# Kernel optimization log

Hardware: AMD Instinct MI355X
Metric: run time of the kernel (lower is better)

## Reference

```python
import jax, jax.numpy as jnp
import numpy as np

E = 1024  # embed_dim
H = 16    # heads
D = E // H            # head_dim = 64
M = 4 * D             # nb_features = 256
B, N = 4, 4096
KERNEL_EPS = 1e-4


def setup_inputs() -> dict:
    key = jax.random.key(0)
    ks = jax.random.split(key, 7)
    s = E ** -0.5
    return {
        "x": jax.random.normal(ks[0], (B, N, E), jnp.float32),
        "Wq": jax.random.normal(ks[1], (E, E), jnp.float32) * s,
        "bq": jnp.zeros((E,), jnp.float32),
        "Wk": jax.random.normal(ks[2], (E, E), jnp.float32) * s,
        "bk": jnp.zeros((E,), jnp.float32),
        "Wv": jax.random.normal(ks[3], (E, E), jnp.float32) * s,
        "bv": jnp.zeros((E,), jnp.float32),
        "Wo": jax.random.normal(ks[4], (E, E), jnp.float32) * s,
        "bo": jnp.zeros((E,), jnp.float32),
        "proj": jax.random.normal(ks[5], (M, D), jnp.float32),  # FAVOR+ random features
    }


def softmax_kernel(data, proj, is_query):
    # data: [B,H,N,D], proj: [M,D] -> features [B,H,N,M]
    d = data.shape[-1]
    data_n = data * (d ** -0.25)
    ratio = proj.shape[0] ** -0.5
    dd = jnp.einsum('bhnd,md->bhnm', data_n, proj)
    diag = 0.5 * jnp.sum(data_n * data_n, axis=-1, keepdims=True)
    if is_query:
        stab = jnp.max(dd, axis=-1, keepdims=True)
    else:
        stab = jnp.max(dd)
    return ratio * (jnp.exp(dd - diag - stab) + KERNEL_EPS)


def reference(x, Wq, bq, Wk, bk, Wv, bv, Wo, bo, proj):
    b, n, e = x.shape
    def split_heads(t):
        return t.reshape(b, n, H, D).transpose(0, 2, 1, 3)  # [B,H,N,D]
    q = split_heads(x @ Wq.T + bq)
    k = split_heads(x @ Wk.T + bk)
    v = split_heads(x @ Wv.T + bv)

    qf = softmax_kernel(q, proj, is_query=True)   # [B,H,N,M]
    kf = softmax_kernel(k, proj, is_query=False)  # [B,H,N,M]

    # non-causal linear attention: O(N*M*D)
    k_sum = jnp.sum(kf, axis=-2)                          # [B,H,M]
    d_inv = 1.0 / jnp.einsum('bhnm,bhm->bhn', qf, k_sum)  # [B,H,N]
    context = jnp.einsum('bhnm,bhnd->bhmd', kf, v)        # [B,H,M,D]
    out = jnp.einsum('bhnm,bhmd,bhn->bhnd', qf, context, d_inv)

    out = out.transpose(0, 2, 1, 3).reshape(b, n, e)
    return out @ Wo.T + bo
```

## Files before the change

### kernel.cpp

```cpp
#include <hip/hip_runtime.h>
#include <hip/hip_bf16.h>
#include <stdint.h>


#define TOKN  16384
#define SEQ   4096
#define EMB   1024
#define LDQ   3072
#define NHEAD 16
#define HD    64
#define NF    256
#define BHN   64

static __device__ __forceinline__ constexpr float c1f()  { return 0.35355339059327379f; }
static __device__ __forceinline__ constexpr float ratf() { return 0.0625f; }
static __device__ __forceinline__ constexpr float kepsf(){ return 1e-4f; }

typedef unsigned short u16;
typedef unsigned int   u32;
typedef __attribute__((ext_vector_type(8))) short bf16x8;
typedef __attribute__((ext_vector_type(4))) float f32x4;
typedef __attribute__((ext_vector_type(4))) u16   u16x4;

union U8 { bf16x8 v8; u16x4 q[2]; };

__device__ __forceinline__ float bf2f(u16 u) { return __uint_as_float(((u32)u) << 16); }
__device__ __forceinline__ u16 f2bf(float f) {
  u32 u = __float_as_uint(f);
  u += 0x7fffu + ((u >> 16) & 1u);
  return (u16)(u >> 16);
}
__device__ __forceinline__ u32 encf(float f) {
  u32 u = __float_as_uint(f);
  return (u & 0x80000000u) ? ~u : (u | 0x80000000u);
}
__device__ __forceinline__ float decf(u32 e) {
  u32 u = (e & 0x80000000u) ? (e & 0x7fffffffu) : ~e;
  return __uint_as_float(u);
}

__device__ __forceinline__ void gl2lds16(const u16* g, void* l) {
  __builtin_amdgcn_global_load_lds(
      (const __attribute__((address_space(1))) u32*)g,
      (__attribute__((address_space(3))) u32*)l, 16, 0, 0);
}

#define ZERO_ACC(acc)                         \
  _Pragma("unroll") for (int _i = 0; _i < 4; _i++) \
  _Pragma("unroll") for (int _j = 0; _j < 4; _j++) acc[_i][_j] = (f32x4)0.0f;

template <int BM, int BN>
__device__ __forceinline__ void gemm_core(const u16* __restrict__ Ag, long lda,
                                          const u16* __restrict__ Bg, long ldb,
                                          int K, u16* sA, u16* sB,
                                          f32x4 (&acc)[4][4]) {
  const int tid = threadIdx.x;
  const int w = tid >> 6, l = tid & 63;
  constexpr int WM = BM / 64;
  const int wm = w % WM, wn = w / WM;
  const int lrow = l & 15, g4 = l >> 4;
  constexpr int AI = (BM * 8) / 256;
  constexpr int BI = (BN * 8) / 256;

  for (int k0 = 0; k0 < K; k0 += 64) {
    __syncthreads();
#pragma unroll
    for (int i = 0; i < AI; i++) {
      int q = i * 256 + tid;
      int row = q >> 3, part = (q & 7) ^ (row & 7);
      gl2lds16(Ag + (long)row * lda + k0 + part * 8,
               (char*)sA + i * 4096 + w * 1024);
    }
#pragma unroll
    for (int i = 0; i < BI; i++) {
      int q = i * 256 + tid;
      int row = q >> 3, part = (q & 7) ^ (row & 7);
      gl2lds16(Bg + (long)row * ldb + k0 + part * 8,
               (char*)sB + i * 4096 + w * 1024);
    }
    __syncthreads();
#pragma unroll
    for (int kk = 0; kk < 2; kk++) {
      bf16x8 af[4], bfr[4];
#pragma unroll
      for (int mt = 0; mt < 4; mt++) {
        int row = wm * 64 + mt * 16 + lrow;
        af[mt] = *(const bf16x8*)(sA + row * 64 + (((kk * 4 + g4) ^ (row & 7)) * 8));
      }
#pragma unroll
      for (int nt = 0; nt < 4; nt++) {
        int row = wn * 64 + nt * 16 + lrow;
        bfr[nt] = *(const bf16x8*)(sB + row * 64 + (((kk * 4 + g4) ^ (row & 7)) * 8));
      }
#pragma unroll
      for (int mt = 0; mt < 4; mt++)
#pragma unroll
        for (int nt = 0; nt < 4; nt++)
          acc[mt][nt] = __builtin_amdgcn_mfma_f32_16x16x32_bf16(af[mt], bfr[nt], acc[mt][nt], 0, 0, 0);
    }
  }
}

template <bool BF16OUT>
__global__ __launch_bounds__(256) void k_gemm(const u16* __restrict__ A, const u16* __restrict__ Bw,
                                              void* __restrict__ Cout, const float* __restrict__ bias,
                                              int K, int lda, int ldb, int ldc) {
  __shared__ __align__(16) u16 sA[128 * 64];
  __shared__ __align__(16) u16 sB[128 * 64];
  const int nbx = gridDim.x;
  const int nwg = nbx * gridDim.y;
  int lin = blockIdx.y * nbx + blockIdx.x;
  if ((nwg & 7) == 0) {
    int per = nwg >> 3;
    lin = (lin & 7) * per + (lin >> 3);
  }
  const int m0 = (lin / nbx) * 128, n0 = (lin % nbx) * 128;
  f32x4 acc[4][4]; ZERO_ACC(acc);
  gemm_core<128, 128>(A + (long)m0 * lda, lda, Bw + (long)n0 * ldb, ldb, K, sA, sB, acc);
  const int l = threadIdx.x & 63, w = threadIdx.x >> 6;
  const int wm = w & 1, wn = w >> 1, lr4 = (l >> 4) * 4, lc = l & 15;
#pragma unroll
  for (int nt = 0; nt < 4; nt++) {
    int gcol = n0 + wn * 64 + nt * 16 + lc;
    float bia = bias[gcol];
#pragma unroll
    for (int mt = 0; mt < 4; mt++)
#pragma unroll
      for (int r = 0; r < 4; r++) {
        int grow = m0 + wm * 64 + mt * 16 + lr4 + r;
        float v = acc[mt][nt][r] + bia;
        if (BF16OUT) ((u16*)Cout)[(long)grow * ldc + gcol] = f2bf(v);
        else         ((float*)Cout)[(long)grow * ldc + gcol] = v;
      }
  }
}

__global__ __launch_bounds__(256) void k_gemm3(const u16* __restrict__ A, const u16* __restrict__ Bw,
                                               u16* __restrict__ Cout,
                                               const float* __restrict__ b0, const float* __restrict__ b1,
                                               const float* __restrict__ b2,
                                               int K, int lda, int ldb, int ldc) {
  __shared__ __align__(16) u16 sA[128 * 64];
  __shared__ __align__(16) u16 sB[128 * 64];
  const int nbx = gridDim.x;
  const int nwg = nbx * gridDim.y;
  int lin = blockIdx.y * nbx + blockIdx.x;
  if ((nwg & 7) == 0) {
    int per = nwg >> 3;
    lin = (lin & 7) * per + (lin >> 3);
  }
  const int m0 = (lin / nbx) * 128, n0 = (lin % nbx) * 128;
  f32x4 acc[4][4]; ZERO_ACC(acc);
  gemm_core<128, 128>(A + (long)m0 * lda, lda, Bw + (long)n0 * ldb, ldb, K, sA, sB, acc);
  const int l = threadIdx.x & 63, w = threadIdx.x >> 6;
  const int wm = w & 1, wn = w >> 1, lr4 = (l >> 4) * 4, lc = l & 15;
  const int seg = n0 >> 10;
  const float* bias = seg == 0 ? b0 : (seg == 1 ? b1 : b2);
#pragma unroll
  for (int nt = 0; nt < 4; nt++) {
    int gcol = n0 + wn * 64 + nt * 16 + lc;
    float bia = bias[gcol & 1023];
#pragma unroll
    for (int mt = 0; mt < 4; mt++)
#pragma unroll
      for (int r = 0; r < 4; r++) {
        int grow = m0 + wm * 64 + mt * 16 + lr4 + r;
        Cout[(long)grow * ldc + gcol] = f2bf(acc[mt][nt][r] + bia);
      }
  }
}

__global__ __launch_bounds__(256) void k_vT(const u16* __restrict__ vb, u16* __restrict__ vT,
                                            float* __restrict__ vsum) {
  __shared__ u16 t[64][72];
  const int bh = blockIdx.y, n0 = blockIdx.x * 64, b = bh >> 4, h = bh & 15;
  const int tid = threadIdx.x;
#pragma unroll
  for (int i = 0; i < 2; i++) {
    int idx = i * 256 + tid, row = idx >> 3, c8 = idx & 7;
    U8 u;
    u.v8 = *(const bf16x8*)&vb[((long)(b * SEQ) + n0 + row) * LDQ + h * HD + c8 * 8];
    *(u16x4*)&t[row][c8 * 8]     = u.q[0];
    *(u16x4*)&t[row][c8 * 8 + 4] = u.q[1];
  }
  __syncthreads();
  const int nq = tid & 15, dh = tid >> 4;
#pragma unroll
  for (int i = 0; i < 4; i++) {
    int d = i * 16 + dh;
    u16x4 pk; float s = 0.f;
#pragma unroll
    for (int j = 0; j < 4; j++) { u16 v = t[nq * 4 + j][d]; pk[j] = v; s += bf2f(v); }
    *(u16x4*)&vT[((long)bh * HD + d) * SEQ + n0 + nq * 4] = pk;
    s += __shfl_xor(s, 1); s += __shfl_xor(s, 2);
    s += __shfl_xor(s, 4); s += __shfl_xor(s, 8);
    if (nq == 0) atomicAdd(&vsum[bh * HD + d], s);
  }
}

__global__ __launch_bounds__(256, 2) void k_fk_ctx(const u16* __restrict__ kb, const u16* __restrict__ vT,
                                                   const u16* __restrict__ projb, u16* __restrict__ part,
                                                   float* __restrict__ su, u32* __restrict__ stabEnc) {
  __shared__ __align__(16) u16 sU[4][64 * 64];
  const int ck = blockIdx.x, bh = blockIdx.y, b = bh >> 4, h = bh & 15;
  const int tid = threadIdx.x, w = tid >> 6, l = tid & 63;
  const int c = l & 15, g = l >> 4;
  u16* sUw = &sU[w][0];
  const int sw = c & 7;

  bf16x8 pf[4][2];
#pragma unroll
  for (int nt = 0; nt < 4; nt++)
#pragma unroll
    for (int k0 = 0; k0 < 2; k0++)
      pf[nt][k0] = *(const bf16x8*)&projb[(w * 64 + nt * 16 + c) * 64 + k0 * 32 + g * 8];

  f32x4 acc2[4][4]; ZERO_ACC(acc2);
  float suv[4] = {0.f, 0.f, 0.f, 0.f};
  float amax = -1e30f;
  const long tok0 = (long)b * SEQ + ck * 256;

  for (int s = 0; s < 4; s++) {
    const long t0 = tok0 + s * 64;
    bf16x8 af[4][2];
#pragma unroll
    for (int mt = 0; mt < 4; mt++)
#pragma unroll
      for (int k0 = 0; k0 < 2; k0++)
        af[mt][k0] = *(const bf16x8*)&kb[(t0 + mt * 16 + c) * LDQ + h * HD + k0 * 32 + g * 8];
    bf16x8 vf[2][4];
#pragma unroll
    for (int k0 = 0; k0 < 2; k0++)
#pragma unroll
      for (int nt = 0; nt < 4; nt++)
        vf[k0][nt] = *(const bf16x8*)&vT[((long)bh * HD + nt * 16 + c) * SEQ +
                                         ck * 256 + s * 64 + k0 * 32 + g * 8];

#pragma unroll
    for (int mt = 0; mt < 4; mt++) {
      float ss = 0.f;
#pragma unroll
      for (int k0 = 0; k0 < 2; k0++)
#pragma unroll
        for (int j = 0; j < 8; j++) {
          float v = bf2f((u16)af[mt][k0][j]);
          ss += v * v;
        }
      ss += __shfl_xor(ss, 16);
      ss += __shfl_xor(ss, 32);
      const float dgrow = ss * 0.0625f;
      f32x4 accR[4];
#pragma unroll
      for (int nt = 0; nt < 4; nt++) accR[nt] = (f32x4)0.0f;
#pragma unroll
      for (int k0 = 0; k0 < 2; k0++)
#pragma unroll
        for (int nt = 0; nt < 4; nt++)
          accR[nt] = __builtin_amdgcn_mfma_f32_16x16x32_bf16(af[mt][k0], pf[nt][k0], accR[nt], 0, 0, 0);
      float dg[4];
#pragma unroll
      for (int r = 0; r < 4; r++) dg[r] = __shfl(dgrow, g * 4 + r);
#pragma unroll
      for (int nt = 0; nt < 4; nt++) {
        u16x4 pk;
#pragma unroll
        for (int r = 0; r < 4; r++) {
          float a = accR[nt][r];
          amax = fmaxf(amax, a);
          float U = __expf(fmaf(a, c1f(), -dg[r]));
          pk[r] = f2bf(U);
          suv[nt] += U;
        }
        *(u16x4*)&sUw[(nt * 16 + c) * 64 + (((mt * 2 + (g >> 1)) ^ sw) * 2 + (g & 1)) * 4] = pk;
      }
    }
#pragma unroll
    for (int k0 = 0; k0 < 2; k0++) {
      bf16x8 uf[4];
#pragma unroll
      for (int mt = 0; mt < 4; mt++)
        uf[mt] = *(const bf16x8*)&sUw[(mt * 16 + c) * 64 + ((k0 * 4 + g) ^ sw) * 8];
#pragma unroll
      for (int mt = 0; mt < 4; mt++)
#pragma unroll
        for (int nt = 0; nt < 4; nt++)
          acc2[mt][nt] = __builtin_amdgcn_mfma_f32_16x16x32_bf16(uf[mt], vf[k0][nt], acc2[mt][nt], 0, 0, 0);
    }
  }
  const long zp = (long)(bh * 16 + ck);
#pragma unroll
  for (int mt = 0; mt < 4; mt++)
#pragma unroll
    for (int nt = 0; nt < 4; nt++)
#pragma unroll
      for (int r = 0; r < 4; r++) {
        int m = w * 64 + mt * 16 + g * 4 + r;
        int d = nt * 16 + c;
        part[(zp * NF + m) * HD + d] = f2bf(acc2[mt][nt][r]);
      }
#pragma unroll
  for (int nt = 0; nt < 4; nt++) {
    float v = suv[nt];
    v += __shfl_xor(v, 16);
    v += __shfl_xor(v, 32);
    if (l < 16) atomicAdd(&su[bh * NF + w * 64 + nt * 16 + l], v);
  }
  for (int o = 32; o; o >>= 1) amax = fmaxf(amax, __shfl_xor(amax, o));
  if (l == 0) atomicMax(stabEnc, encf(c1f() * amax));
}

__global__ __launch_bounds__(256, 4) void k_fq_attn(const u16* __restrict__ qb, const u16* __restrict__ projb,
                                                    const float* __restrict__ k_sum, const float* __restrict__ ksum_tot,
                                                    const u16* __restrict__ ct_bf, const float* __restrict__ ctsum,
                                                    u16* __restrict__ attn_bf) {
  __shared__ __align__(16) u16 sUq[64 * 256];
  __shared__ float redmax[4][64];
  __shared__ float redsum[4][64];
  const int bh = blockIdx.y, b = bh >> 4, h = bh & 15;
  const long t0 = (long)b * SEQ + blockIdx.x * 64;
  const int tid = threadIdx.x, w = tid >> 6, l = tid & 63;
  const int lrow = l & 15, lk = (l >> 4) * 8, lr4 = (l >> 4) * 4, lc = l & 15;

  bf16x8 pf[4][2];
#pragma unroll
  for (int mt = 0; mt < 4; mt++)
#pragma unroll
    for (int k0 = 0; k0 < 2; k0++)
      pf[mt][k0] = *(const bf16x8*)&projb[(w * 64 + mt * 16 + lrow) * 64 + k0 * 32 + lk];
  bf16x8 af[4][2];
#pragma unroll
  for (int nt = 0; nt < 4; nt++)
#pragma unroll
    for (int k0 = 0; k0 < 2; k0++)
      af[nt][k0] = *(const bf16x8*)&qb[(t0 + nt * 16 + lrow) * LDQ + h * HD + k0 * 32 + lk];

  float dgq[4];
#pragma unroll
  for (int nt = 0; nt < 4; nt++) {
    float ss = 0.f;
#pragma unroll
    for (int k0 = 0; k0 < 2; k0++)
#pragma unroll
      for (int j = 0; j < 8; j++) {
        float v = bf2f((u16)af[nt][k0][j]);
        ss += v * v;
      }
    ss += __shfl_xor(ss, 16);
    ss += __shfl_xor(ss, 32);
    dgq[nt] = ss * 0.0625f;
  }

  f32x4 ksr[4];
#pragma unroll
  for (int mt = 0; mt < 4; mt++)
    ksr[mt] = *(const f32x4*)&k_sum[(long)bh * NF + w * 64 + mt * 16 + lr4];

#pragma unroll
  for (int nt = 0; nt < 4; nt++) {
    f32x4 accC[4];
#pragma unroll
    for (int mt = 0; mt < 4; mt++) accC[mt] = (f32x4)0.0f;
#pragma unroll
    for (int k0 = 0; k0 < 2; k0++)
#pragma unroll
      for (int mt = 0; mt < 4; mt++)
        accC[mt] = __builtin_amdgcn_mfma_f32_16x16x32_bf16(pf[mt][k0], af[nt][k0], accC[mt], 0, 0, 0);

    const int tok = nt * 16 + lc;
    const int trow = tok * NF, tsw = tok & 7;
    float vmax = -1e30f, s = 0.f;
#pragma unroll
    for (int mt = 0; mt < 4; mt++) {
      const int fb = w * 64 + mt * 16 + lr4;
      u16x4 pk;
#pragma unroll
      for (int r = 0; r < 4; r++) {
        float dd = c1f() * accC[mt][r];
        vmax = fmaxf(vmax, dd);
        float U = __expf(dd - dgq[nt]);
        pk[r] = f2bf(U);
        s += U * ksr[mt][r];
      }
      *(u16x4*)&sUq[trow + (((fb >> 3) ^ tsw) << 3) + (fb & 7)] = pk;
    }
    vmax = fmaxf(vmax, __shfl_xor(vmax, 16));
    vmax = fmaxf(vmax, __shfl_xor(vmax, 32));
    s += __shfl_xor(s, 16);
    s += __shfl_xor(s, 32);
    if (l < 16) { redmax[w][nt * 16 + l] = vmax; redsum[w][nt * 16 + l] = s; }
  }
  __syncthreads();
  f32x4 acc2[4];
#pragma unroll
  for (int mt = 0; mt < 4; mt++) acc2[mt] = (f32x4)0.0f;
#pragma unroll
  for (int kk = 0; kk < 8; kk++) {
    bf16x8 bfr = *(const bf16x8*)&ct_bf[((long)bh * HD + w * 16 + lrow) * NF + kk * 32 + lk];
#pragma unroll
    for (int mt = 0; mt < 4; mt++) {
      int row = mt * 16 + lrow;
      bf16x8 a2 = *(const bf16x8*)&sUq[row * NF + (((kk * 4 + (l >> 4)) ^ (row & 7)) * 8)];
      acc2[mt] = __builtin_amdgcn_mfma_f32_16x16x32_bf16(a2, bfr, acc2[mt], 0, 0, 0);
    }
  }
  const float kst = ksum_tot[bh];
  const float cts = ctsum[(long)bh * HD + w * 16 + lc];
#pragma unroll
  for (int mt = 0; mt < 4; mt++)
#pragma unroll
    for (int r = 0; r < 4; r++) {
      int row = mt * 16 + lr4 + r;
      float rs = fmaxf(fmaxf(redmax[0][row], redmax[1][row]),
                       fmaxf(redmax[2][row], redmax[3][row]));
      float S1 = redsum[0][row] + redsum[1][row] + redsum[2][row] + redsum[3][row];
      float ers = __expf(-rs);
      float di = 1.0f / (ratf() * (ers * S1 + kepsf() * kst));
      float a_ = di * ratf() * ers;
      float b_ = di * ratf() * kepsf();
      float ov = a_ * acc2[mt][r] + b_ * cts;
      attn_bf[(t0 + row) * EMB + h * HD + w * 16 + lc] = f2bf(ov);
    }
}

__global__ void k_cvt(const float* __restrict__ s, u16* __restrict__ d, long n4) {
  long i = (long)blockIdx.x * blockDim.x + threadIdx.x;
  if (i >= n4) return;
  float4 v = ((const float4*)s)[i];
  u16x4 o = { f2bf(v.x), f2bf(v.y), f2bf(v.z), f2bf(v.w) };
  ((u16x4*)d)[i] = o;
}

__global__ void k_init(float* su, float* vsum, u32* stabEnc) {
  int i = blockIdx.x * 256 + threadIdx.x;
  if (i < BHN * NF) su[i] = 0.f;
  if (i < BHN * HD) vsum[i] = 0.f;
  if (i == 0) *stabEnc = 0u;
}

__global__ __launch_bounds__(256) void k_asm_ksum(const float* __restrict__ su, const u32* __restrict__ stabEnc,
                                                  float* __restrict__ k_sum, float* __restrict__ ksum_tot) {
  __shared__ float red[256];
  int z = blockIdx.x, m = threadIdx.x;
  float es = __expf(-decf(*stabEnc));
  float v = ratf() * (es * su[(long)z * NF + m] + kepsf() * (float)SEQ);
  k_sum[(long)z * NF + m] = v;
  red[m] = v;
  __syncthreads();
  for (int s = 128; s > 0; s >>= 1) {
    if (m < s) red[m] += red[m + s];
    __syncthreads();
  }
  if (m == 0) ksum_tot[z] = red[0];
}

__global__ __launch_bounds__(256) void k_asm_ct(const u16* __restrict__ part, const float* __restrict__ vsum,
                                                const u32* __restrict__ stabEnc, u16* __restrict__ ct_bf,
                                                float* __restrict__ ctsum) {
  __shared__ float red[4][64];
  const int z = blockIdx.x, tid = threadIdx.x;
  const int w = tid >> 6, l = tid & 63;
  float es = __expf(-decf(*stabEnc));
  float vs = vsum[(long)z * HD + l];
  float csum = 0.f;
  for (int m = w; m < NF; m += 4) {
    float a = 0.f;
#pragma unroll
    for (int ck = 0; ck < 16; ck++)
      a += bf2f(part[((long)(z * 16 + ck) * NF + m) * HD + l]);
    float cv = ratf() * (es * a + kepsf() * vs);
    ct_bf[((long)z * HD + l) * NF + m] = f2bf(cv);
    csum += cv;
  }
  red[w][l] = csum;
  __syncthreads();
  if (tid < 64)
    ctsum[(long)z * HD + tid] = red[0][tid] + red[1][tid] + red[2][tid] + red[3][tid];
}

extern "C" void kernel_launch(void* const* d_in, const int* in_sizes, int n_in,
                              void* d_out, int out_size, void* d_ws, size_t ws_size,
                              hipStream_t stream) {
  const float* x    = (const float*)d_in[0];
  const float* Wq   = (const float*)d_in[1];
  const float* bq   = (const float*)d_in[2];
  const float* Wk   = (const float*)d_in[3];
  const float* bk   = (const float*)d_in[4];
  const float* Wv   = (const float*)d_in[5];
  const float* bv   = (const float*)d_in[6];
  const float* Wo   = (const float*)d_in[7];
  const float* bo   = (const float*)d_in[8];
  const float* proj = (const float*)d_in[9];

  char* base = (char*)d_ws;
  size_t off = 0;
  auto alloc = [&](size_t bytes) {
    off = (off + 255) & ~(size_t)255;
    char* r = base + off;
    off += bytes;
    return r;
  };
  u16*  xb     = (u16*)alloc((size_t)TOKN * EMB * 2);
  u16*  wqkv   = (u16*)alloc((size_t)3 * EMB * EMB * 2);
  u16*  wob    = (u16*)alloc((size_t)EMB * EMB * 2);
  u16*  projb  = (u16*)alloc((size_t)NF * HD * 2);
  u16*  qkv    = (u16*)alloc((size_t)TOKN * LDQ * 2);
  float* su    = (float*)alloc((size_t)BHN * NF * 4);
  float* k_sum = (float*)alloc((size_t)BHN * NF * 4);
  float* ksum_t= (float*)alloc((size_t)BHN * 4);
  float* vsum  = (float*)alloc((size_t)BHN * HD * 4);
  float* ctsum = (float*)alloc((size_t)BHN * HD * 4);
  u32*  stabE  = (u32*)alloc(256);
  u16*  ct_bf  = (u16*)alloc((size_t)BHN * HD * NF * 2);
  u16*  qb     = qkv;
  u16*  kb     = qkv + EMB;
  u16*  vb     = qkv + 2 * EMB;
  u16*  part   = xb;
  u16*  attn_bf= xb;
  u16*  vT     = (u16*)d_out;

  k_init<<<64, 256, 0, stream>>>(su, vsum, stabE);
  k_cvt<<<(TOKN * EMB / 4 + 255) / 256, 256, 0, stream>>>(x, xb, (long)TOKN * EMB / 4);
  k_cvt<<<(EMB * EMB / 4 + 255) / 256, 256, 0, stream>>>(Wq, wqkv, (long)EMB * EMB / 4);
  k_cvt<<<(EMB * EMB / 4 + 255) / 256, 256, 0, stream>>>(Wk, wqkv + (size_t)EMB * EMB, (long)EMB * EMB / 4);
  k_cvt<<<(EMB * EMB / 4 + 255) / 256, 256, 0, stream>>>(Wv, wqkv + (size_t)2 * EMB * EMB, (long)EMB * EMB / 4);
  k_cvt<<<(EMB * EMB / 4 + 255) / 256, 256, 0, stream>>>(Wo, wob, (long)EMB * EMB / 4);
  k_cvt<<<(NF * HD / 4 + 255) / 256, 256, 0, stream>>>(proj, projb, (long)NF * HD / 4);
  k_gemm3<<<dim3(LDQ / 128, TOKN / 128), 256, 0, stream>>>(xb, wqkv, qkv, bq, bk, bv,
                                                           EMB, EMB, EMB, LDQ);
  k_vT<<<dim3(SEQ / 64, BHN), 256, 0, stream>>>(vb, vT, vsum);
  k_fk_ctx<<<dim3(16, BHN), 256, 0, stream>>>(kb, vT, projb, part, su, stabE);
  k_asm_ksum<<<BHN, 256, 0, stream>>>(su, stabE, k_sum, ksum_t);
  k_asm_ct<<<BHN, 256, 0, stream>>>(part, vsum, stabE, ct_bf, ctsum);
  k_fq_attn<<<dim3(SEQ / 64, BHN), 256, 0, stream>>>(qb, projb, k_sum, ksum_t, ct_bf, ctsum, attn_bf);
  k_gemm<false><<<dim3(EMB / 128, TOKN / 128), 256, 0, stream>>>(attn_bf, wob, d_out, bo, EMB, EMB, EMB, EMB);
}
```

Before: 513.0 us.

## Double-buffer GEMM shared-memory tiles to overlap global loads with MFMA

Converts the GEMM main loop to a two-stage LDS ping-pong: the next K-tile is issued with direct global-to-LDS loads while the current tile is consumed by MFMAs, synchronized through explicit vmcnt waits and s_barrier. This hides global-load latency that previously stalled each iteration between two syncthreads. LDS per block doubles to 64KB, which can reduce occupancy, and the hardcoded vmcnt(8) depends on exactly eight loads per thread per tile.

Result: faster. 501.9 us (-2.2%).

```diff
diff --git a/kernel.cpp b/kernel.cpp
--- a/kernel.cpp
+++ b/kernel.cpp
@@ -61,36 +61,53 @@
   const int lrow = l & 15, g4 = l >> 4;
   constexpr int AI = (BM * 8) / 256;
   constexpr int BI = (BN * 8) / 256;
-
-  for (int k0 = 0; k0 < K; k0 += 64) {
-    __syncthreads();
+  static_assert(AI + BI == 8, "vmcnt(8) literal assumes 8 loads/thread/tile");
+  constexpr int ABUF = BM * 64;
+  constexpr int BBUF = BN * 64;
+
+  auto stage = [&](int k0, int sel) {
 #pragma unroll
     for (int i = 0; i < AI; i++) {
       int q = i * 256 + tid;
       int row = q >> 3, part = (q & 7) ^ (row & 7);
       gl2lds16(Ag + (long)row * lda + k0 + part * 8,
-               (char*)sA + i * 4096 + w * 1024);
+               (char*)(sA + sel * ABUF) + i * 4096 + w * 1024);
     }
 #pragma unroll
     for (int i = 0; i < BI; i++) {
       int q = i * 256 + tid;
       int row = q >> 3, part = (q & 7) ^ (row & 7);
       gl2lds16(Bg + (long)row * ldb + k0 + part * 8,
-               (char*)sB + i * 4096 + w * 1024);
-    }
-    __syncthreads();
+               (char*)(sB + sel * BBUF) + i * 4096 + w * 1024);
+    }
+  };
+
+  stage(0, 0);
+  const int NT = K >> 6;
+  for (int t = 0; t < NT; ++t) {
+    const int sel = t & 1;
+    if (t + 1 < NT) {
+      stage((t + 1) * 64, sel ^ 1);
+      asm volatile("s_waitcnt vmcnt(8)" ::: "memory");
+    } else {
+      asm volatile("s_waitcnt vmcnt(0)" ::: "memory");
+    }
+    __builtin_amdgcn_s_barrier();
+    __builtin_amdgcn_sched_barrier(0);
+    const u16* pA = sA + sel * ABUF;
+    const u16* pB = sB + sel * BBUF;
 #pragma unroll
     for (int kk = 0; kk < 2; kk++) {
       bf16x8 af[4], bfr[4];
 #pragma unroll
       for (int mt = 0; mt < 4; mt++) {
         int row = wm * 64 + mt * 16 + lrow;
-        af[mt] = *(const bf16x8*)(sA + row * 64 + (((kk * 4 + g4) ^ (row & 7)) * 8));
+        af[mt] = *(const bf16x8*)(pA + row * 64 + (((kk * 4 + g4) ^ (row & 7)) * 8));
       }
 #pragma unroll
       for (int nt = 0; nt < 4; nt++) {
         int row = wn * 64 + nt * 16 + lrow;
-        bfr[nt] = *(const bf16x8*)(sB + row * 64 + (((kk * 4 + g4) ^ (row & 7)) * 8));
+        bfr[nt] = *(const bf16x8*)(pB + row * 64 + (((kk * 4 + g4) ^ (row & 7)) * 8));
       }
 #pragma unroll
       for (int mt = 0; mt < 4; mt++)
@@ -98,6 +115,7 @@
         for (int nt = 0; nt < 4; nt++)
           acc[mt][nt] = __builtin_amdgcn_mfma_f32_16x16x32_bf16(af[mt], bfr[nt], acc[mt][nt], 0, 0, 0);
     }
+    __builtin_amdgcn_s_barrier();
   }
 }
 
@@ -105,8 +123,8 @@
 __global__ __launch_bounds__(256) void k_gemm(const u16* __restrict__ A, const u16* __restrict__ Bw,
                                               void* __restrict__ Cout, const float* __restrict__ bias,
                                               int K, int lda, int ldb, int ldc) {
-  __shared__ __align__(16) u16 sA[128 * 64];
-  __shared__ __align__(16) u16 sB[128 * 64];
+  __shared__ __align__(16) u16 sA[2 * 128 * 64];
+  __shared__ __align__(16) u16 sB[2 * 128 * 64];
   const int nbx = gridDim.x;
   const int nwg = nbx * gridDim.y;
   int lin = blockIdx.y * nbx + blockIdx.x;
@@ -140,8 +158,8 @@
                                                const float* __restrict__ b0, const float* __restrict__ b1,
                                                const float* __restrict__ b2,
                                                int K, int lda, int ldb, int ldc) {
-  __shared__ __align__(16) u16 sA[128 * 64];
-  __shared__ __align__(16) u16 sB[128 * 64];
+  __shared__ __align__(16) u16 sA[2 * 128 * 64];
+  __shared__ __align__(16) u16 sB[2 * 128 * 64];
   const int nbx = gridDim.x;
   const int nwg = nbx * gridDim.y;
   int lin = blockIdx.y * nbx + blockIdx.x;
```
